# Kernel optimization log

Measured on AMD Instinct MI355X. Metric: run time of the kernel, lower is better.

## Reference

```python
import jax, jax.numpy as jnp
import numpy as np

C = 64   # input_channels
H = 128  # hidden_channels


def setup_inputs() -> dict:
    key = jax.random.key(0)
    ks = jax.random.split(key, 13)
    s = lambda k, shape, fan_in: jax.random.uniform(k, shape, jnp.float32, -1.0, 1.0) / np.sqrt(fan_in)
    return {
        "x": jax.random.normal(ks[0], (2, 512, C), jnp.float32),
        "Wa": s(ks[1], (C, H), C),  "ba": s(ks[2], (H,), C),
        "Wb": s(ks[3], (H, H), H), "bb": s(ks[4], (H,), H),
        "Wc1": s(ks[5], (H, H), H), "bc1": s(ks[6], (H,), H),
        "Wc2": s(ks[7], (H, H), H), "bc2": s(ks[8], (H,), H),
        "Wc3": s(ks[9], (H, H), H), "bc3": s(ks[10], (H,), H),
        "Wo": s(ks[11], (H, 1), H), "bo": s(ks[12], (1,), H),
    }


def reference(x, Wa, ba, Wb, bb, Wc1, bc1, Wc2, bc2, Wc3, bc3, Wo, bo):
    B, N, _ = x.shape
    # node MLP
    h = jax.nn.relu(jnp.einsum("bnc,ch->bnh", x, Wa) + ba)
    h = jax.nn.relu(jnp.einsum("bnh,hk->bnk", h, Wb) + bb)
    # pairwise difference: diff[b,i,j] = h[b,j] - h[b,i]  (matches x_a - x_b)
    d = h[:, None, :, :] - h[:, :, None, :]  # [B,N,N,H]
    e = jax.nn.relu(jnp.einsum("bijh,hk->bijk", d, Wc1) + bc1)
    e = jax.nn.relu(jnp.einsum("bijh,hk->bijk", e, Wc2) + bc2)
    e = jax.nn.relu(jnp.einsum("bijh,hk->bijk", e, Wc3) + bc3)
    out = jnp.einsum("bijh,ho->bijo", e, Wo) + bo  # [B,N,N,1]
    return out[..., 0]  # [B,N,N]
```

## Files before the change

kernel.cpp:

```cpp
#include <hip/hip_runtime.h>


typedef _Float16 half_t;
typedef __attribute__((ext_vector_type(2))) _Float16 f16x2;
typedef __attribute__((ext_vector_type(8))) _Float16 f16x8;
typedef __attribute__((ext_vector_type(4))) float f32x4;


__global__ __launch_bounds__(256) void prep_kernel(
    const float* __restrict__ x, const float* __restrict__ Wa, const float* __restrict__ ba,
    const float* __restrict__ Wb, const float* __restrict__ bb, const float* __restrict__ Wc1,
    const float* __restrict__ bc1, const float* __restrict__ Wc2, const float* __restrict__ Wc3,
    half_t* __restrict__ gh, half_t* __restrict__ gbh,
    half_t* __restrict__ W2T, half_t* __restrict__ W3T)
{
  const int t = threadIdx.x;
  if (blockIdx.x >= 256) {
    const int bid = blockIdx.x - 256;
    const int layer = bid >> 3, nt = bid & 7;
    const int ks = t >> 6, L = t & 63, q = L >> 4, cc = L & 15;
    const float* src = layer ? Wc3 : Wc2;
    half_t* dst = layer ? W3T : W2T;
    f16x8 v;
    #pragma unroll
    for (int e = 0; e < 8; e++)
      v[e] = (half_t)src[(32 * ks + 8 * q + e) * 128 + 16 * nt + cc];
    *(f16x8*)(dst + (nt * 4 + ks) * 512 + L * 8) = v;
    return;
  }
  __shared__ float sx[64 * 6];
  __shared__ float sh1[128 * 6];
  __shared__ float sh2[128 * 6];
  const int n0 = blockIdx.x * 4;
  const int col = t & 127, hf = t >> 7;

  sx[(t & 63) * 6 + (t >> 6)] = x[(n0 + (t >> 6)) * 64 + (t & 63)];
  __syncthreads();

  float a0 = ba[col], a1 = a0;
  #pragma unroll
  for (int cc = 0; cc < 64; cc++) {
    const float wv = Wa[cc * 128 + col];
    const float2 xv = *(const float2*)(sx + cc * 6 + hf * 2);
    a0 = fmaf(xv.x, wv, a0); a1 = fmaf(xv.y, wv, a1);
  }
  *(float2*)(sh1 + col * 6 + hf * 2) = make_float2(fmaxf(a0, 0.f), fmaxf(a1, 0.f));
  __syncthreads();

  float b0 = bb[col], b1 = b0;
  #pragma unroll
  for (int k = 0; k < 128; k++) {
    const float wv = Wb[k * 128 + col];
    const float2 hv = *(const float2*)(sh1 + k * 6 + hf * 2);
    b0 = fmaf(hv.x, wv, b0); b1 = fmaf(hv.y, wv, b1);
  }
  *(float2*)(sh2 + col * 6 + hf * 2) = make_float2(fmaxf(b0, 0.f), fmaxf(b1, 0.f));
  __syncthreads();

  float c0 = 0.f, c1 = 0.f;
  #pragma unroll
  for (int k = 0; k < 128; k++) {
    const float wv = Wc1[k * 128 + col];
    const float2 hv = *(const float2*)(sh2 + k * 6 + hf * 2);
    c0 = fmaf(hv.x, wv, c0); c1 = fmaf(hv.y, wv, c1);
  }
  const float bv = bc1[col];
  const int r0 = n0 + hf * 2;
  gh [(r0 + 0) * 128 + col] = (half_t)c0;
  gh [(r0 + 1) * 128 + col] = (half_t)c1;
  gbh[(r0 + 0) * 128 + col] = (half_t)(c0 + bv);
  gbh[(r0 + 1) * 128 + col] = (half_t)(c1 + bv);
}

static __device__ inline f16x8 relu_sub8(f16x8 a, f16x8 b) {
  f16x8 d = a - b;
  const f16x8 z = {};
  return __builtin_elementwise_max(d, z);
}

__global__ __launch_bounds__(512)
void edge_kernel(
    const half_t* __restrict__ gh, const half_t* __restrict__ gbh,
    const half_t* __restrict__ W2T, const half_t* __restrict__ W3T,
    const float* __restrict__ bc2, const float* __restrict__ bc3,
    const float* __restrict__ Wo, const float* __restrict__ bo,
    float* __restrict__ out)
{
  __shared__ __align__(16) half_t sW2[16384];
  __shared__ __align__(16) half_t sE[8 * 8192];

  const int t = threadIdx.x, lane = t & 63, w = t >> 6;
  const int c = lane & 15, q = lane >> 4;
  const int bid = blockIdx.x;
  const int b = bid >> 7, ic = bid & 127;
  const int i0 = ic * 4;
  const int j0 = w * 64;

  #pragma unroll
  for (int k = 0; k < 4; k++) {
    const int off = (k * 512 + t) * 8;
    *(f16x8*)(sW2 + off) = *(const f16x8*)(W2T + off);
  }
  __syncthreads();

  const float bo0 = bo[0];
  const int packoff = ((q >> 1) * 16 + c) * 8 + (q & 1) * 4;
  const int rdoff = lane * 8;
  half_t* sEw = sE + w * 8192;

  #pragma unroll 1
  for (int u = 0; u < 4; u++) {
    const int i = i0 + u;

    f16x8 e1[4][4];
    {
      f16x8 gih[4];
      #pragma unroll
      for (int ks = 0; ks < 4; ks++)
        gih[ks] = *(const f16x8*)(gh + (size_t)(b * 512 + i) * 128 + ks * 32 + q * 8);
      #pragma unroll
      for (int ks = 0; ks < 4; ks++)
        #pragma unroll
        for (int jt = 0; jt < 4; jt++) {
          const f16x8 gj = *(const f16x8*)(gbh + (size_t)(b * 512 + j0 + jt * 16 + c) * 128 + ks * 32 + q * 8);
          e1[ks][jt] = relu_sub8(gj, gih[ks]);
        }
    }

    #pragma unroll 1
    for (int nt = 0; nt < 8; nt++) {
      f16x8 wf[4];
      #pragma unroll
      for (int ks = 0; ks < 4; ks++)
        wf[ks] = *(const f16x8*)(sW2 + (nt * 4 + ks) * 512 + rdoff);
      const f32x4 b2 = *(const f32x4*)(bc2 + nt * 16 + q * 4);
      f32x4 acc[4] = {b2, b2, b2, b2};
      __builtin_amdgcn_s_setprio(1);
      #pragma unroll
      for (int ks = 0; ks < 4; ks++)
        #pragma unroll
        for (int jt = 0; jt < 4; jt++)
          acc[jt] = __builtin_amdgcn_mfma_f32_16x16x32_f16(wf[ks], e1[ks][jt], acc[jt], 0, 0, 0);
      __builtin_amdgcn_s_setprio(0);
      const int po = ((nt >> 1) * 512) + packoff + (nt & 1) * 256;
      #pragma unroll
      for (int jt = 0; jt < 4; jt++) {
        const f32x4 v = acc[jt];
        f16x2 h01, h23;
        h01[0] = (half_t)fmaxf(v[0], 0.f); h01[1] = (half_t)fmaxf(v[1], 0.f);
        h23[0] = (half_t)fmaxf(v[2], 0.f); h23[1] = (half_t)fmaxf(v[3], 0.f);
        uint2 uv;
        uv.x = __builtin_bit_cast(unsigned int, h01);
        uv.y = __builtin_bit_cast(unsigned int, h23);
        *(uint2*)(sEw + jt * 2048 + po) = uv;
      }
    }

    {
      f16x8 be[4][4];
      #pragma unroll
      for (int ks3 = 0; ks3 < 4; ks3++)
        #pragma unroll
        for (int jt = 0; jt < 4; jt++)
          be[ks3][jt] = *(const f16x8*)(sEw + (jt * 4 + ks3) * 512 + rdoff);

      float p[4] = {0.f, 0.f, 0.f, 0.f};
      #pragma unroll 1
      for (int mt = 0; mt < 8; mt++) {
        f16x8 wf[4];
        #pragma unroll
        for (int ks3 = 0; ks3 < 4; ks3++)
          wf[ks3] = *(const f16x8*)(W3T + (mt * 4 + ks3) * 512 + rdoff);
        const f32x4 b3 = *(const f32x4*)(bc3 + mt * 16 + q * 4);
        f32x4 acc[4] = {b3, b3, b3, b3};
        __builtin_amdgcn_s_setprio(1);
        #pragma unroll
        for (int ks3 = 0; ks3 < 4; ks3++)
          #pragma unroll
          for (int jt = 0; jt < 4; jt++)
            acc[jt] = __builtin_amdgcn_mfma_f32_16x16x32_f16(wf[ks3], be[ks3][jt], acc[jt], 0, 0, 0);
        __builtin_amdgcn_s_setprio(0);
        const f32x4 wo = *(const f32x4*)(Wo + mt * 16 + q * 4);
        #pragma unroll
        for (int jt = 0; jt < 4; jt++)
          #pragma unroll
          for (int rr = 0; rr < 4; rr++)
            p[jt] = fmaf(fmaxf(acc[jt][rr], 0.f), wo[rr], p[jt]);
      }

      #pragma unroll
      for (int jt = 0; jt < 4; jt++) {
        p[jt] += __shfl_xor(p[jt], 16, 64);
        p[jt] += __shfl_xor(p[jt], 32, 64);
      }
      if (q == 0) {
        const size_t base = ((size_t)(b * 512 + i)) * 512 + j0;
        #pragma unroll
        for (int jt = 0; jt < 4; jt++)
          out[base + jt * 16 + c] = p[jt] + bo0;
      }
    }
  }
}

extern "C" void kernel_launch(void* const* d_in, const int* in_sizes, int n_in,
                              void* d_out, int out_size, void* d_ws, size_t ws_size,
                              hipStream_t stream)
{
  const float* x   = (const float*)d_in[0];
  const float* Wa  = (const float*)d_in[1];
  const float* ba  = (const float*)d_in[2];
  const float* Wb  = (const float*)d_in[3];
  const float* bb  = (const float*)d_in[4];
  const float* Wc1 = (const float*)d_in[5];
  const float* bc1 = (const float*)d_in[6];
  const float* Wc2 = (const float*)d_in[7];
  const float* bc2 = (const float*)d_in[8];
  const float* Wc3 = (const float*)d_in[9];
  const float* bc3 = (const float*)d_in[10];
  const float* Wo  = (const float*)d_in[11];
  const float* bo  = (const float*)d_in[12];
  float* out = (float*)d_out;

  char* ws = (char*)d_ws;
  half_t* gh  = (half_t*)ws;
  half_t* gbh = (half_t*)(ws + 262144);
  half_t* W2T = (half_t*)(ws + 524288);
  half_t* W3T = (half_t*)(ws + 557056);

  prep_kernel<<<272, 256, 0, stream>>>(x, Wa, ba, Wb, bb, Wc1, bc1, Wc2, Wc3,
                                       gh, gbh, W2T, W3T);
  edge_kernel<<<256, 512, 0, stream>>>(gh, gbh, W2T, W3T, bc2, bc3, Wo, bo, out);
}
```

Measured before the change: 122.6 us.

## Double-buffer W3 fragment loads, stagger waves, and move bias add to epilogue

The layer-3 loop now processes two output tiles per iteration and prefetches the next W3 weight fragments from global memory while the current MFMAs run, hiding load latency. Bias adds for layers 2 and 3 move from accumulator initialisation into the ReLU epilogue, so the accumulators start at zero and the bias load is issued earlier. Half the waves sleep briefly after the prologue to stagger their phases so MFMA and memory work from different waves overlap. The extra register buffers raise register pressure, and the sleep adds fixed latency.

```diff
diff --git a/kernel.cpp b/kernel.cpp
--- a/kernel.cpp
+++ b/kernel.cpp
@@ -103,6 +103,8 @@
   }
   __syncthreads();
 
+  if (w >= 4) __builtin_amdgcn_s_sleep(64);
+
   const float bo0 = bo[0];
   const int packoff = ((q >> 1) * 16 + c) * 8 + (q & 1) * 4;
   const int rdoff = lane * 8;
@@ -129,12 +131,12 @@
 
     #pragma unroll 1
     for (int nt = 0; nt < 8; nt++) {
+      const f32x4 b2 = *(const f32x4*)(bc2 + nt * 16 + q * 4);
       f16x8 wf[4];
       #pragma unroll
       for (int ks = 0; ks < 4; ks++)
         wf[ks] = *(const f16x8*)(sW2 + (nt * 4 + ks) * 512 + rdoff);
-      const f32x4 b2 = *(const f32x4*)(bc2 + nt * 16 + q * 4);
-      f32x4 acc[4] = {b2, b2, b2, b2};
+      f32x4 acc[4] = {};
       __builtin_amdgcn_s_setprio(1);
       #pragma unroll
       for (int ks = 0; ks < 4; ks++)
@@ -147,8 +149,8 @@
       for (int jt = 0; jt < 4; jt++) {
         const f32x4 v = acc[jt];
         f16x2 h01, h23;
-        h01[0] = (half_t)fmaxf(v[0], 0.f); h01[1] = (half_t)fmaxf(v[1], 0.f);
-        h23[0] = (half_t)fmaxf(v[2], 0.f); h23[1] = (half_t)fmaxf(v[3], 0.f);
+        h01[0] = (half_t)fmaxf(v[0] + b2[0], 0.f); h01[1] = (half_t)fmaxf(v[1] + b2[1], 0.f);
+        h23[0] = (half_t)fmaxf(v[2] + b2[2], 0.f); h23[1] = (half_t)fmaxf(v[3] + b2[3], 0.f);
         uint2 uv;
         uv.x = __builtin_bit_cast(unsigned int, h01);
         uv.y = __builtin_bit_cast(unsigned int, h23);
@@ -164,28 +166,55 @@
         for (int jt = 0; jt < 4; jt++)
           be[ks3][jt] = *(const f16x8*)(sEw + (jt * 4 + ks3) * 512 + rdoff);
 
+      f16x8 wfa[4], wfb[4];
+      #pragma unroll
+      for (int ks3 = 0; ks3 < 4; ks3++)
+        wfa[ks3] = *(const f16x8*)(W3T + ks3 * 512 + rdoff);
+
       float p[4] = {0.f, 0.f, 0.f, 0.f};
       #pragma unroll 1
-      for (int mt = 0; mt < 8; mt++) {
-        f16x8 wf[4];
+      for (int mp = 0; mp < 4; mp++) {
+        const int ma = mp * 2, mb = ma + 1;
         #pragma unroll
         for (int ks3 = 0; ks3 < 4; ks3++)
-          wf[ks3] = *(const f16x8*)(W3T + (mt * 4 + ks3) * 512 + rdoff);
-        const f32x4 b3 = *(const f32x4*)(bc3 + mt * 16 + q * 4);
-        f32x4 acc[4] = {b3, b3, b3, b3};
-        __builtin_amdgcn_s_setprio(1);
+          wfb[ks3] = *(const f16x8*)(W3T + (mb * 4 + ks3) * 512 + rdoff);
+        {
+          const f32x4 b3 = *(const f32x4*)(bc3 + ma * 16 + q * 4);
+          const f32x4 wo = *(const f32x4*)(Wo  + ma * 16 + q * 4);
+          f32x4 acc[4] = {};
+          __builtin_amdgcn_s_setprio(1);
+          #pragma unroll
+          for (int ks3 = 0; ks3 < 4; ks3++)
+            #pragma unroll
+            for (int jt = 0; jt < 4; jt++)
+              acc[jt] = __builtin_amdgcn_mfma_f32_16x16x32_f16(wfa[ks3], be[ks3][jt], acc[jt], 0, 0, 0);
+          __builtin_amdgcn_s_setprio(0);
+          #pragma unroll
+          for (int jt = 0; jt < 4; jt++)
+            #pragma unroll
+            for (int rr = 0; rr < 4; rr++)
+              p[jt] = fmaf(fmaxf(acc[jt][rr] + b3[rr], 0.f), wo[rr], p[jt]);
+        }
         #pragma unroll
         for (int ks3 = 0; ks3 < 4; ks3++)
+          wfa[ks3] = *(const f16x8*)(W3T + (((ma + 2) & 7) * 4 + ks3) * 512 + rdoff);
+        {
+          const f32x4 b3 = *(const f32x4*)(bc3 + mb * 16 + q * 4);
+          const f32x4 wo = *(const f32x4*)(Wo  + mb * 16 + q * 4);
+          f32x4 acc[4] = {};
+          __builtin_amdgcn_s_setprio(1);
+          #pragma unroll
+          for (int ks3 = 0; ks3 < 4; ks3++)
+            #pragma unroll
+            for (int jt = 0; jt < 4; jt++)
+              acc[jt] = __builtin_amdgcn_mfma_f32_16x16x32_f16(wfb[ks3], be[ks3][jt], acc[jt], 0, 0, 0);
+          __builtin_amdgcn_s_setprio(0);
           #pragma unroll
           for (int jt = 0; jt < 4; jt++)
-            acc[jt] = __builtin_amdgcn_mfma_f32_16x16x32_f16(wf[ks3], be[ks3][jt], acc[jt], 0, 0, 0);
-        __builtin_amdgcn_s_setprio(0);
-        const f32x4 wo = *(const f32x4*)(Wo + mt * 16 + q * 4);
-        #pragma unroll
-        for (int jt = 0; jt < 4; jt++)
-          #pragma unroll
-          for (int rr = 0; rr < 4; rr++)
-            p[jt] = fmaf(fmaxf(acc[jt][rr], 0.f), wo[rr], p[jt]);
+            #pragma unroll
+            for (int rr = 0; rr < 4; rr++)
+              p[jt] = fmaf(fmaxf(acc[jt][rr] + b3[rr], 0.f), wo[rr], p[jt]);
+        }
       }
 
       #pragma unroll
```

Measured after the change: 121.8 us. No clear change (-0.6%).
